# Kernel optimization log

Measured on AMD Instinct MI355X. Metric: run time of the kernel, lower is better.

The kernel has to match this reference:

```python
import jax, jax.numpy as jnp
import numpy as np

IMG, P, C = 512, 16, 1
D, DEPTH, H, DH, MLP = 768, 12, 8, 64, 2048
GRID = IMG // P          # 32
NP = GRID * GRID         # 1024 patches
N = NP + 1               # +cls token
EPS = 1e-5


def _ln(x, s, b):
    m = jnp.mean(x, -1, keepdims=True)
    v = jnp.mean((x - m) ** 2, -1, keepdims=True)
    return (x - m) * jax.lax.rsqrt(v + EPS) * s + b


def setup_inputs() -> dict:
    key = jax.random.key(0)
    ks = jax.random.split(key, 12)
    s = 0.02
    f32 = jnp.float32
    return {
        "x": jax.random.normal(ks[0], (4, C, IMG, IMG), f32),
        "conv_w": jax.random.normal(ks[1], (D, C, P, P), f32) * s,   # [out,in,kh,kw] like torch
        "conv_b": jnp.zeros((D,), f32),
        "cls_token": jax.random.normal(ks[2], (1, 1, D), f32),
        "pos_emb": jax.random.normal(ks[3], (1, N, D), f32),
        "qkv_w": jax.random.normal(ks[4], (DEPTH, D, 3 * H * DH), f32) * s,  # [in,out] layout
        "merge_w": jax.random.normal(ks[5], (DEPTH, H * DH, D), f32) * s,
        "merge_b": jnp.zeros((DEPTH, D), f32),
        "ln1_s": jnp.ones((DEPTH, D), f32),
        "ln1_b": jnp.zeros((DEPTH, D), f32),
        "ln2_s": jnp.ones((DEPTH, D), f32),
        "ln2_b": jnp.zeros((DEPTH, D), f32),
        "ffn_w1": jax.random.normal(ks[6], (DEPTH, D, MLP), f32) * s,
        "ffn_b1": jnp.zeros((DEPTH, MLP), f32),
        "ffn_w2": jax.random.normal(ks[7], (DEPTH, MLP, D), f32) * s,
        "ffn_b2": jnp.zeros((DEPTH, D), f32),
        "lnf_s": jnp.ones((D,), f32),
        "lnf_b": jnp.zeros((D,), f32),
    }


def reference(x, conv_w, conv_b, cls_token, pos_emb, qkv_w, merge_w, merge_b,
              ln1_s, ln1_b, ln2_s, ln2_b, ffn_w1, ffn_b1, ffn_w2, ffn_b2,
              lnf_s, lnf_b):
    B = x.shape[0]
    # Patch embed: stride-P conv == non-overlapping patch extraction + matmul
    xr = x.reshape(B, C, GRID, P, GRID, P)
    tok = jnp.einsum('bchpwq,dcpq->bhwd', xr, conv_w).reshape(B, NP, D) + conv_b
    t = jnp.concatenate([jnp.broadcast_to(cls_token, (B, 1, D)), tok], axis=1)
    t = t + pos_emb  # dropout is identity in eval
    scale = DH ** -0.5
    for i in range(DEPTH):
        # MSA with pre-LN
        h = _ln(t, ln1_s[i], ln1_b[i])
        qkv = (h @ qkv_w[i]).reshape(B, N, H, 3, DH)   # [B,N,H,3,DH]
        q = jnp.transpose(qkv[..., 0, :], (0, 2, 1, 3))  # [B,H,N,DH]
        k = jnp.transpose(qkv[..., 1, :], (0, 2, 1, 3))
        v = jnp.transpose(qkv[..., 2, :], (0, 2, 1, 3))
        att = jax.nn.softmax(jnp.einsum('bhnd,bhmd->bhnm', q, k) * scale, axis=-1)
        o = jnp.einsum('bhnm,bhmd->bhnd', att, v)
        o = jnp.transpose(o, (0, 2, 1, 3)).reshape(B, N, H * DH)
        t = t + (o @ merge_w[i] + merge_b[i])
        # FFN with pre-LN, exact (erf) GELU like torch nn.GELU
        h2 = _ln(t, ln2_s[i], ln2_b[i])
        f = jax.nn.gelu(h2 @ ffn_w1[i] + ffn_b1[i], approximate=False)
        t = t + (f @ ffn_w2[i] + ffn_b2[i])
    return _ln(t, lnf_s, lnf_b)
```

## Files before the change

kernel.cpp:

```cpp
#include <hip/hip_runtime.h>

#define DEV __device__ __forceinline__

typedef short s8v __attribute__((ext_vector_type(8)));
typedef float f4v __attribute__((ext_vector_type(4)));
typedef unsigned int u32x2 __attribute__((ext_vector_type(2)));

DEV short f2bf(float f) {
  unsigned u = __float_as_uint(f);
  u += 0x7FFFu + ((u >> 16) & 1u);
  return (short)(u >> 16);
}
DEV short f2bf_fast(float f) {
  return (short)((__float_as_uint(f) + 0x8000u) >> 16);
}
DEV float bf2f(short s) { return __uint_as_float(((unsigned)(unsigned short)s) << 16); }

DEV void gld_lds16(const short* g, short* l) {
  __builtin_amdgcn_global_load_lds(
      (const __attribute__((address_space(1))) void*)g,
      (__attribute__((address_space(3))) void*)l, 16, 0, 0);
}

DEV u32x2 trr(unsigned lds_byte) {
  u32x2 r;
  asm volatile("ds_read_b64_tr_b16 %0, %1" : "=&v"(r) : "v"(lds_byte));
  return r;
}

DEV int xcd_swz(int id, int nwg) {
  int q8 = nwg >> 3, r8 = nwg & 7, xcd = id & 7, off = id >> 3;
  return (xcd < r8) ? (xcd * (q8 + 1) + off) : (r8 * (q8 + 1) + (xcd - r8) * q8 + off);
}

template<int BN>
__global__ __launch_bounds__(256) void gemm_t(
    const short* __restrict__ A, const short* __restrict__ B, void* __restrict__ Cv,
    const float* __restrict__ bias,
    int M, int N, int K, int lda, int ldb, int ldc, int flags)
{
  constexpr int BPASS = BN / 32;
  constexpr int MI = (BN == 128) ? 4 : 2;
  __shared__ __align__(16) short As[2][64 * 64];
  __shared__ __align__(16) short Bs[2][BN * 64];
  int nwg = gridDim.x * gridDim.y;
  int idl = blockIdx.y * gridDim.x + blockIdx.x;
  int swz = xcd_swz(idl, nwg);
  int bx = swz % gridDim.x, by = swz / gridDim.x;
  int m0 = by * 64, n0 = bx * BN;
  int tid = threadIdx.x, lane = tid & 63, w = tid >> 6;
  int lr = lane & 15, kg = lane >> 4;
  int wrb = (BN == 128) ? 0 : (w >> 1) * 32;
  int wcb = (BN == 128) ? w * 32 : (w & 1) * 32;
  f4v acc[MI][2] = {};
  int NT = K >> 6;

#define STAGE(bufi, k0)                                                   \
  {                                                                       \
    _Pragma("unroll")                                                     \
    for (int p = 0; p < 2; ++p) {                                         \
      int ch = p * 256 + w * 64 + lane;                                   \
      int row = ch >> 3, c = (ch & 7) ^ (row & 7);                        \
      gld_lds16(A + (long)(m0 + row) * lda + (k0) + c * 8,                \
                &As[bufi][(p * 256 + w * 64) * 8]);                       \
    }                                                                     \
    _Pragma("unroll")                                                     \
    for (int p = 0; p < BPASS; ++p) {                                     \
      int ch = p * 256 + w * 64 + lane;                                   \
      int row = ch >> 3, c = (ch & 7) ^ (row & 7);                        \
      gld_lds16(B + (long)(n0 + row) * ldb + (k0) + c * 8,                \
                &Bs[bufi][(p * 256 + w * 64) * 8]);                       \
    }                                                                     \
  }

  STAGE(0, 0)
  for (int t = 0; t < NT; ++t) {
    int buf = t & 1;
    if (t + 1 < NT) {
      STAGE(buf ^ 1, (t + 1) * 64)
      if constexpr (BN == 128)
        asm volatile("s_waitcnt vmcnt(6)" ::: "memory");
      else
        asm volatile("s_waitcnt vmcnt(4)" ::: "memory");
    } else {
      asm volatile("s_waitcnt vmcnt(0)" ::: "memory");
    }
    __builtin_amdgcn_s_barrier();
    #pragma unroll
    for (int ks = 0; ks < 2; ++ks) {
      s8v av[MI], bv[2];
      #pragma unroll
      for (int mi = 0; mi < MI; ++mi) {
        int row = wrb + mi * 16 + lr;
        int sl = (ks * 4 + kg) ^ (row & 7);
        av[mi] = *(const s8v*)&As[buf][row * 64 + sl * 8];
      }
      #pragma unroll
      for (int ni = 0; ni < 2; ++ni) {
        int row = wcb + ni * 16 + lr;
        int sl = (ks * 4 + kg) ^ (row & 7);
        bv[ni] = *(const s8v*)&Bs[buf][row * 64 + sl * 8];
      }
      #pragma unroll
      for (int mi = 0; mi < MI; ++mi)
        #pragma unroll
        for (int ni = 0; ni < 2; ++ni)
          acc[mi][ni] = __builtin_amdgcn_mfma_f32_16x16x32_bf16(av[mi], bv[ni], acc[mi][ni], 0, 0, 0);
    }
    asm volatile("s_waitcnt lgkmcnt(0)" ::: "memory");
    __builtin_amdgcn_s_barrier();
  }
#undef STAGE

  float* Cf = (float*)Cv;
  short* Cb = (short*)Cv;
  #pragma unroll
  for (int mi = 0; mi < MI; ++mi)
    #pragma unroll
    for (int ni = 0; ni < 2; ++ni) {
      int col = n0 + wcb + ni * 16 + lr;
      float bvv = (flags & 1) ? bias[col] : 0.f;
      #pragma unroll
      for (int j = 0; j < 4; ++j) {
        int row = m0 + wrb + mi * 16 + kg * 4 + j;
        if (row >= M) continue;
        float v = acc[mi][ni][j] + bvv;
        if (flags & 2) v = 0.5f * v * (1.f + erff(v * 0.70710678118f));
        long ci = (long)row * ldc + col;
        if (flags & 8) Cb[ci] = f2bf(v);
        else { if (flags & 4) v += Cf[ci]; Cf[ci] = v; }
      }
    }
}

__global__ __launch_bounds__(256) void flash_k(
    const short* __restrict__ qkv, float* __restrict__ Opart, float* __restrict__ ML)
{
  int swz = xcd_swz(blockIdx.x, 1088);
  int h = swz / 544, rem = swz - h * 544;
  int z = rem / 17, qt = rem - z * 17;
  int zb = z >> 3, zh = z & 7;
  const short* base = qkv + (long)zb * 1025 * 1536 + zh * 192;
  const short* Qg = base;
  const short* Kg = base + 64;
  const short* Vg = base + 128;
  int q0 = qt * 64;
  int kt0 = h * 8;
  int tid = threadIdx.x, lane = tid & 63, w = tid >> 6;
  int lr = lane & 15, kg = lane >> 4;

  __shared__ __align__(16) short Ks[2][64 * 64];
  __shared__ __align__(16) short Vs[2][64 * 64];

  s8v aq[2];
  {
    long qrow = q0 + w * 16 + lr;
    aq[0] = *(const s8v*)(Qg + qrow * 1536 + kg * 8);
    aq[1] = *(const s8v*)(Qg + qrow * 1536 + 32 + kg * 8);
  }

  unsigned vsbase = (unsigned)(unsigned long long)
      (__attribute__((address_space(3))) void*)&Vs[0][0];
  unsigned vtr = (unsigned)(lr * 8 + kg * 1024);

#define STAGE_K(bufi, kv0)                                                 \
  {                                                                        \
    int s0 = w * 128;                                                      \
    _Pragma("unroll")                                                      \
    for (int i = 0; i < 2; ++i) {                                          \
      int s = s0 + i * 64 + lane;                                          \
      int row = s >> 3, c = (s & 7) ^ (row & 7);                           \
      gld_lds16(Kg + (long)((kv0) + row) * 1536 + c * 8,                   \
                &Ks[bufi][(s0 + i * 64) * 8]);                             \
    }                                                                      \
  }
#define STAGE_V(bufi, kv0)                                                 \
  {                                                                        \
    int s0 = w * 128;                                                      \
    _Pragma("unroll")                                                      \
    for (int i = 0; i < 2; ++i) {                                          \
      int ch = s0 + i * 64 + lane;                                         \
      int st = ch >> 3, r = (ch & 7) >> 1, hh = ch & 1;                    \
      int key = (kv0) + (st >> 2) * 4 + r;                                 \
      int d = (st & 3) * 16 + hh * 8;                                      \
      gld_lds16(Vg + (long)key * 1536 + d,                                 \
                &Vs[bufi][(s0 + i * 64) * 8]);                             \
    }                                                                      \
  }

  f4v acc[4] = {};
  float m_run = -3.0e38f, l_run = 0.f;
  const float C2 = 0.18033688011112042f;
  const float THR = 44.36f;

  STAGE_K(0, kt0 * 64)
  STAGE_V(0, kt0 * 64)
  asm volatile("s_waitcnt vmcnt(0)" ::: "memory");
  __builtin_amdgcn_s_barrier();

  for (int kt = kt0; kt < kt0 + 8; ++kt) {
    int cur = (kt - kt0) & 1;
    if (kt + 1 < kt0 + 8) {
      STAGE_K(cur ^ 1, (kt + 1) * 64)
      STAGE_V(cur ^ 1, (kt + 1) * 64)
    }

    f4v sa[4] = {};
    __builtin_amdgcn_s_setprio(1);
    #pragma unroll
    for (int ni = 0; ni < 4; ++ni) {
      int row = ni * 16 + lr;
      #pragma unroll
      for (int ks = 0; ks < 2; ++ks) {
        int c = (ks * 4 + kg) ^ (row & 7);
        s8v kf = *(const s8v*)&Ks[cur][row * 64 + c * 8];
        sa[ni] = __builtin_amdgcn_mfma_f32_16x16x32_bf16(kf, aq[ks], sa[ni], 0, 0, 0);
      }
    }
    __builtin_amdgcn_s_setprio(0);

    float tm = -3.0e38f;
    #pragma unroll
    for (int ni = 0; ni < 4; ++ni)
      #pragma unroll
      for (int jj = 0; jj < 4; ++jj) tm = fmaxf(tm, sa[ni][jj]);
    tm = fmaxf(tm, __shfl_xor(tm, 16));
    tm = fmaxf(tm, __shfl_xor(tm, 32));
    bool need = !__all(tm <= m_run + THR);
    float scale = 1.f;
    if (need) {
      float m_new = fmaxf(m_run, tm);
      scale = exp2f((m_run - m_new) * C2);
      m_run = m_new;
    }
    float mC = m_run * C2;
    float pv[4][4];
    float ts = 0.f;
    #pragma unroll
    for (int ni = 0; ni < 4; ++ni)
      #pragma unroll
      for (int jj = 0; jj < 4; ++jj) {
        float p = exp2f(fmaf(sa[ni][jj], C2, -mC));
        pv[ni][jj] = p;
        ts += p;
      }
    ts += __shfl_xor(ts, 16);
    ts += __shfl_xor(ts, 32);
    l_run = l_run * scale + ts;
    if (need) {
      float scq[4];
      #pragma unroll
      for (int jj = 0; jj < 4; ++jj)
        scq[jj] = __shfl(scale, kg * 4 + jj + 16 * kg);
      #pragma unroll
      for (int ni = 0; ni < 4; ++ni)
        #pragma unroll
        for (int jj = 0; jj < 4; ++jj) acc[ni][jj] *= scq[jj];
    }

    unsigned pr[4][2];
    #pragma unroll
    for (int ni = 0; ni < 4; ++ni)
      #pragma unroll
      for (int hh = 0; hh < 2; ++hh) {
        unsigned lo = (unsigned)(unsigned short)f2bf_fast(pv[ni][2 * hh]);
        unsigned hi = (unsigned)(unsigned short)f2bf_fast(pv[ni][2 * hh + 1]);
        pr[ni][hh] = lo | (hi << 16);
      }
    union PU { s8v v; unsigned u[4]; };
    PU apu[2];
    #pragma unroll
    for (int ks = 0; ks < 2; ++ks)
      #pragma unroll
      for (int t = 0; t < 4; ++t) {
        unsigned src = (kg & 2) ? pr[2 * ks + 1][t & 1] : pr[2 * ks][t & 1];
        apu[ks].u[t] = __shfl(src, lr + 16 * (2 * (kg & 1) + (t >> 1)));
      }

    u32x2 tr[4][2][2];
    unsigned vb = vsbase + (unsigned)cur * 8192u + vtr;
    #pragma unroll
    for (int ni = 0; ni < 4; ++ni)
      #pragma unroll
      for (int ks = 0; ks < 2; ++ks) {
        tr[ni][ks][0] = trr(vb + ni * 128 + ks * 4096);
        tr[ni][ks][1] = trr(vb + ni * 128 + ks * 4096 + 512);
      }
    asm volatile("s_waitcnt lgkmcnt(0)" ::: "memory");
    __builtin_amdgcn_sched_barrier(0);

    __builtin_amdgcn_s_setprio(1);
    #pragma unroll
    for (int ni = 0; ni < 4; ++ni) {
      #pragma unroll
      for (int ks = 0; ks < 2; ++ks) {
        union { s8v v; u32x2 u2[2]; } bb;
        bb.u2[0] = tr[ni][ks][0];
        bb.u2[1] = tr[ni][ks][1];
        acc[ni] = __builtin_amdgcn_mfma_f32_16x16x32_bf16(apu[ks].v, bb.v, acc[ni], 0, 0, 0);
      }
    }
    __builtin_amdgcn_s_setprio(0);
    asm volatile("s_waitcnt lgkmcnt(0)" ::: "memory");
    asm volatile("s_waitcnt vmcnt(0)" ::: "memory");
    __builtin_amdgcn_s_barrier();
  }
#undef STAGE_K
#undef STAGE_V

  if (h) {
    s8v k0 = *(const s8v*)(Kg + 1024L * 1536 + kg * 8);
    s8v k1 = *(const s8v*)(Kg + 1024L * 1536 + 32 + kg * 8);
    float s = 0.f;
    #pragma unroll
    for (int j = 0; j < 8; ++j)
      s += bf2f(aq[0][j]) * bf2f(k0[j]) + bf2f(aq[1][j]) * bf2f(k1[j]);
    s += __shfl_xor(s, 16);
    s += __shfl_xor(s, 32);
    float m_new = fmaxf(m_run, s);
    float sc = exp2f((m_run - m_new) * C2);
    float p = exp2f((s - m_new) * C2);
    m_run = m_new;
    l_run = l_run * sc + p;
    float vrow[4];
    #pragma unroll
    for (int ni = 0; ni < 4; ++ni)
      vrow[ni] = bf2f(Vg[1024L * 1536 + ni * 16 + lr]);
    float scq[4], pq[4];
    #pragma unroll
    for (int jj = 0; jj < 4; ++jj) {
      scq[jj] = __shfl(sc, kg * 4 + jj + 16 * kg);
      pq[jj]  = __shfl(p,  kg * 4 + jj + 16 * kg);
    }
    #pragma unroll
    for (int ni = 0; ni < 4; ++ni)
      #pragma unroll
      for (int jj = 0; jj < 4; ++jj)
        acc[ni][jj] = acc[ni][jj] * scq[jj] + pq[jj] * vrow[ni];
  }

  long zrow = (long)(h * 32 + z) * 1025;
  if (kg == 0) {
    int row = q0 + w * 16 + lr;
    if (row < 1025) {
      ML[(zrow + row) * 2]     = m_run * C2;
      ML[(zrow + row) * 2 + 1] = l_run;
    }
  }
  #pragma unroll
  for (int ni = 0; ni < 4; ++ni)
    #pragma unroll
    for (int jj = 0; jj < 4; ++jj) {
      int row = q0 + w * 16 + kg * 4 + jj;
      if (row < 1025)
        Opart[(zrow + row) * 64 + ni * 16 + lr] = acc[ni][jj];
    }
}

__global__ __launch_bounds__(256) void fcomb_k(
    const float* __restrict__ Opart, const float* __restrict__ ML, short* __restrict__ O)
{
  int idx = blockIdx.x * 256 + threadIdx.x;
  int d = idx & 63;
  int r = idx >> 6;
  int z = r / 1025, row = r - z * 1025;
  float m0 = ML[(long)r * 2], l0 = ML[(long)r * 2 + 1];
  float m1 = ML[(long)(32800 + r) * 2], l1 = ML[(long)(32800 + r) * 2 + 1];
  float M = fmaxf(m0, m1);
  float w0 = exp2f(m0 - M), w1 = exp2f(m1 - M);
  float inv = 1.f / (l0 * w0 + l1 * w1);
  float v = (Opart[(long)r * 64 + d] * w0 + Opart[(long)(32800 + r) * 64 + d] * w1) * inv;
  int zb = z >> 3, zh = z & 7;
  O[((long)(zb * 1025 + row)) * 512 + zh * 64 + d] = f2bf(v);
}

DEV void tconv_body(const float* w, short* wt, int K, int N, int bx, int by, int tid)
{
  __shared__ float tile[32][33];
  int n0 = bx * 32, k0 = by * 32;
  int tx = tid & 31, ty = tid >> 5;
  #pragma unroll
  for (int j = 0; j < 4; ++j)
    tile[ty + j * 8][tx] = w[(long)(k0 + ty + j * 8) * N + n0 + tx];
  __syncthreads();
  #pragma unroll
  for (int j = 0; j < 4; ++j)
    wt[(long)(n0 + ty + j * 8) * K + k0 + tx] = f2bf(tile[tx][ty + j * 8]);
}

__global__ __launch_bounds__(256) void tconv4_k(
    const float* __restrict__ sq, const float* __restrict__ sm,
    const float* __restrict__ sf1, const float* __restrict__ sf2,
    short* __restrict__ dq, short* __restrict__ dm,
    short* __restrict__ df1, short* __restrict__ df2)
{
  int id = blockIdx.x, tid = threadIdx.x;
  if (id < 1152)       tconv_body(sq,  dq,  768, 1536, id % 48,          id / 48,          tid);
  else if (id < 1536)  tconv_body(sm,  dm,  512, 768,  (id - 1152) % 24, (id - 1152) / 24, tid);
  else if (id < 3072)  tconv_body(sf1, df1, 768, 2048, (id - 1536) % 64, (id - 1536) / 64, tid);
  else                 tconv_body(sf2, df2, 2048, 768, (id - 3072) % 24, (id - 3072) / 24, tid);
}

__global__ __launch_bounds__(256) void cvt_k(const float* __restrict__ in,
    short* __restrict__ out, int n)
{
  int i = blockIdx.x * 256 + threadIdx.x;
  if (i < n) out[i] = f2bf(in[i]);
}

DEV void st_ln(float* p, float v) { *p = v; }
DEV void st_ln(short* p, float v) { *p = f2bf(v); }

template<typename OT>
__global__ __launch_bounds__(256) void ln_k(const float* __restrict__ x,
    const float* __restrict__ g, const float* __restrict__ b,
    OT* __restrict__ y, int rows)
{
  int row = blockIdx.x;
  if (row >= rows) return;
  const float* xr = x + (long)row * 768;
  OT* yr = y + (long)row * 768;
  int t = threadIdx.x;
  float v0 = xr[t], v1 = xr[t + 256], v2 = xr[t + 512];
  float s = v0 + v1 + v2, s2 = v0 * v0 + v1 * v1 + v2 * v2;
  #pragma unroll
  for (int o = 32; o > 0; o >>= 1) { s += __shfl_down(s, o); s2 += __shfl_down(s2, o); }
  __shared__ float as_[4], as2_[4];
  if ((t & 63) == 0) { as_[t >> 6] = s; as2_[t >> 6] = s2; }
  __syncthreads();
  s = as_[0] + as_[1] + as_[2] + as_[3];
  s2 = as2_[0] + as2_[1] + as2_[2] + as2_[3];
  float mean = s * (1.f / 768.f);
  float var = s2 * (1.f / 768.f) - mean * mean;
  float r = rsqrtf(var + 1e-5f);
  st_ln(&yr[t],       (v0 - mean) * r * g[t]       + b[t]);
  st_ln(&yr[t + 256], (v1 - mean) * r * g[t + 256] + b[t + 256]);
  st_ln(&yr[t + 512], (v2 - mean) * r * g[t + 512] + b[t + 512]);
}

__global__ __launch_bounds__(256) void im2col_k(const float* __restrict__ x,
    short* __restrict__ A)
{
  int i = blockIdx.x * 256 + threadIdx.x;
  int k = i & 255, row = i >> 8;
  int px = k & 15, py = k >> 4;
  int gx = row & 31, gy = (row >> 5) & 31, b = row >> 10;
  A[i] = f2bf(x[((long)(b * 512) + gy * 16 + py) * 512 + gx * 16 + px]);
}

__global__ __launch_bounds__(256) void assemble_k(const short* __restrict__ tok,
    const float* __restrict__ cls, const float* __restrict__ pos, float* __restrict__ t)
{
  int i = blockIdx.x * 256 + threadIdx.x;
  int d = i % 768; int rn = i / 768; int n = rn % 1025; int b = rn / 1025;
  float v = (n == 0) ? cls[d] : bf2f(tok[((long)(b * 1024 + n - 1)) * 768 + d]);
  t[i] = v + pos[n * 768 + d];
}

extern "C" void kernel_launch(void* const* d_in, const int* in_sizes, int n_in,
                              void* d_out, int out_size, void* d_ws, size_t ws_size,
                              hipStream_t stream)
{
  const float* x       = (const float*)d_in[0];
  const float* conv_w  = (const float*)d_in[1];
  const float* conv_b  = (const float*)d_in[2];
  const float* cls     = (const float*)d_in[3];
  const float* pos     = (const float*)d_in[4];
  const float* qkv_w   = (const float*)d_in[5];
  const float* merge_w = (const float*)d_in[6];
  const float* merge_b = (const float*)d_in[7];
  const float* ln1_s   = (const float*)d_in[8];
  const float* ln1_b   = (const float*)d_in[9];
  const float* ln2_s   = (const float*)d_in[10];
  const float* ln2_b   = (const float*)d_in[11];
  const float* ffn_w1  = (const float*)d_in[12];
  const float* ffn_b1  = (const float*)d_in[13];
  const float* ffn_w2  = (const float*)d_in[14];
  const float* ffn_b2  = (const float*)d_in[15];
  const float* lnf_s   = (const float*)d_in[16];
  const float* lnf_b   = (const float*)d_in[17];

  char* wsp = (char*)d_ws;
  size_t o = 0;
  auto take = [&](size_t bytes) { char* r = wsp + o; o = (o + bytes + 255) & ~(size_t)255; return r; };
  short* wq   = (short*)take(1536ul * 768 * 2);
  short* wm   = (short*)take(768ul * 512 * 2);
  short* wf1  = (short*)take(2048ul * 768 * 2);
  short* wf2  = (short*)take(768ul * 2048 * 2);
  short* wcv  = (short*)take(768ul * 256 * 2);
  float* t    = (float*)take(4100ul * 768 * 4);
  char*  hO   = take(4352ul * 768 * 2);
  short* qkv  = (short*)take(4ul * 1025 * 1536 * 2);
  char*  fV   = take(4352ul * 2048 * 2);
  take(2ul << 20);

  short* h     = (short*)hO;
  short* O     = (short*)hO;
  short* f     = (short*)fV;
  short* imc   = (short*)fV;
  short* tok   = (short*)(fV + 4096ul * 256 * 2);
  float* Opart = (float*)fV;
  float* ML    = (float*)(fV + 16793600);

  dim3 blk(256);

  cvt_k<<<768, blk, 0, stream>>>(conv_w, wcv, 768 * 256);
  im2col_k<<<4096, blk, 0, stream>>>(x, imc);
  gemm_t<64><<<dim3(12, 64), blk, 0, stream>>>(imc, wcv, tok, conv_b,
      4096, 768, 256, 256, 256, 768, 1 | 8);
  assemble_k<<<12300, blk, 0, stream>>>(tok, cls, pos, t);

  for (int i = 0; i < 12; ++i) {
    tconv4_k<<<4608, blk, 0, stream>>>(
        qkv_w + (long)i * 768 * 1536, merge_w + (long)i * 512 * 768,
        ffn_w1 + (long)i * 768 * 2048, ffn_w2 + (long)i * 2048 * 768,
        wq, wm, wf1, wf2);

    ln_k<short><<<4100, blk, 0, stream>>>(t, ln1_s + i * 768, ln1_b + i * 768, h, 4100);
    gemm_t<64><<<dim3(24, 65), blk, 0, stream>>>(h, wq, qkv, nullptr,
        4100, 1536, 768, 768, 768, 1536, 8);
    flash_k<<<1088, blk, 0, stream>>>(qkv, Opart, ML);
    fcomb_k<<<8200, blk, 0, stream>>>(Opart, ML, O);
    gemm_t<64><<<dim3(12, 65), blk, 0, stream>>>(O, wm, t, merge_b + i * 768,
        4100, 768, 512, 512, 512, 768, 1 | 4);
    ln_k<short><<<4100, blk, 0, stream>>>(t, ln2_s + i * 768, ln2_b + i * 768, h, 4100);
    gemm_t<64><<<dim3(32, 65), blk, 0, stream>>>(h, wf1, f, ffn_b1 + i * 2048,
        4100, 2048, 768, 768, 768, 2048, 1 | 2 | 8);
    gemm_t<64><<<dim3(12, 65), blk, 0, stream>>>(f, wf2, t, ffn_b2 + i * 768,
        4100, 768, 2048, 2048, 2048, 768, 1 | 4);
  }
  ln_k<float><<<4100, blk, 0, stream>>>(t, lnf_s, lnf_b, (float*)d_out, 4100);
}
```

Measured before the change: 2.034 ms.

## Fuse split-KV flash combine into one 512-thread block; vectorize layernorm per wave

The flash attention kernel now runs both KV halves as two 4-wave groups inside one 512-thread block. The partial accumulators and max/sum statistics are merged through LDS, and bf16 output is written directly. This removes the separate fcomb kernel and the fp32 Opart/ML round-trip through global memory. Separately, layernorm processes one row per wave with float4 loads and shuffle-only reductions, removing the shared-memory barrier. The costs are a doubled LDS footprint per block and an extra block-wide barrier before the combine.

```diff
diff --git a/kernel.cpp b/kernel.cpp
--- a/kernel.cpp
+++ b/kernel.cpp
@@ -2,6 +2,7 @@
 
 #define DEV __device__ __forceinline__
 
+typedef short s4v __attribute__((ext_vector_type(4)));
 typedef short s8v __attribute__((ext_vector_type(8)));
 typedef float f4v __attribute__((ext_vector_type(4)));
 typedef unsigned int u32x2 __attribute__((ext_vector_type(2)));
@@ -133,50 +134,50 @@
     }
 }
 
-__global__ __launch_bounds__(256) void flash_k(
-    const short* __restrict__ qkv, float* __restrict__ Opart, float* __restrict__ ML)
-{
-  int swz = xcd_swz(blockIdx.x, 1088);
-  int h = swz / 544, rem = swz - h * 544;
-  int z = rem / 17, qt = rem - z * 17;
+__global__ __launch_bounds__(512) void flash_k(
+    const short* __restrict__ qkv, short* __restrict__ O)
+{
+  int swz = xcd_swz(blockIdx.x, 544);
+  int z = swz / 17, qt = swz - z * 17;
   int zb = z >> 3, zh = z & 7;
   const short* base = qkv + (long)zb * 1025 * 1536 + zh * 192;
   const short* Qg = base;
   const short* Kg = base + 64;
   const short* Vg = base + 128;
   int q0 = qt * 64;
-  int kt0 = h * 8;
   int tid = threadIdx.x, lane = tid & 63, w = tid >> 6;
+  int g = w >> 2, wl = w & 3;
   int lr = lane & 15, kg = lane >> 4;
-
-  __shared__ __align__(16) short Ks[2][64 * 64];
-  __shared__ __align__(16) short Vs[2][64 * 64];
+  int kt0 = g * 8;
+
+  __shared__ __align__(16) short Ks[2][2][64 * 64];
+  __shared__ __align__(16) short Vs[2][2][64 * 64];
 
   s8v aq[2];
   {
-    long qrow = q0 + w * 16 + lr;
+    long qrow = q0 + wl * 16 + lr;
     aq[0] = *(const s8v*)(Qg + qrow * 1536 + kg * 8);
     aq[1] = *(const s8v*)(Qg + qrow * 1536 + 32 + kg * 8);
   }
 
   unsigned vsbase = (unsigned)(unsigned long long)
-      (__attribute__((address_space(3))) void*)&Vs[0][0];
+      (__attribute__((address_space(3))) void*)&Vs[0][0][0];
   unsigned vtr = (unsigned)(lr * 8 + kg * 1024);
 
 #define STAGE_K(bufi, kv0)                                                 \
   {                                                                        \
-    int s0 = w * 128;                                                      \
+    int s0 = wl * 128;                                                     \
     _Pragma("unroll")                                                      \
     for (int i = 0; i < 2; ++i) {                                          \
       int s = s0 + i * 64 + lane;                                          \
       int row = s >> 3, c = (s & 7) ^ (row & 7);                           \
       gld_lds16(Kg + (long)((kv0) + row) * 1536 + c * 8,                   \
-                &Ks[bufi][(s0 + i * 64) * 8]);                             \
+                &Ks[g][bufi][(s0 + i * 64) * 8]);                          \
     }                                                                      \
   }
 #define STAGE_V(bufi, kv0)                                                 \
   {                                                                        \
-    int s0 = w * 128;                                                      \
+    int s0 = wl * 128;                                                     \
     _Pragma("unroll")                                                      \
     for (int i = 0; i < 2; ++i) {                                          \
       int ch = s0 + i * 64 + lane;                                         \
@@ -184,7 +185,7 @@
       int key = (kv0) + (st >> 2) * 4 + r;                                 \
       int d = (st & 3) * 16 + hh * 8;                                      \
       gld_lds16(Vg + (long)key * 1536 + d,                                 \
-                &Vs[bufi][(s0 + i * 64) * 8]);                             \
+                &Vs[g][bufi][(s0 + i * 64) * 8]);                          \
     }                                                                      \
   }
 
@@ -213,7 +214,7 @@
       #pragma unroll
       for (int ks = 0; ks < 2; ++ks) {
         int c = (ks * 4 + kg) ^ (row & 7);
-        s8v kf = *(const s8v*)&Ks[cur][row * 64 + c * 8];
+        s8v kf = *(const s8v*)&Ks[g][cur][row * 64 + c * 8];
         sa[ni] = __builtin_amdgcn_mfma_f32_16x16x32_bf16(kf, aq[ks], sa[ni], 0, 0, 0);
       }
     }
@@ -278,7 +279,7 @@
       }
 
     u32x2 tr[4][2][2];
-    unsigned vb = vsbase + (unsigned)cur * 8192u + vtr;
+    unsigned vb = vsbase + (unsigned)(g * 2 + cur) * 8192u + vtr;
     #pragma unroll
     for (int ni = 0; ni < 4; ++ni)
       #pragma unroll
@@ -308,7 +309,7 @@
 #undef STAGE_K
 #undef STAGE_V
 
-  if (h) {
+  if (g) {
     s8v k0 = *(const s8v*)(Kg + 1024L * 1536 + kg * 8);
     s8v k1 = *(const s8v*)(Kg + 1024L * 1536 + 32 + kg * 8);
     float s = 0.f;
@@ -339,39 +340,45 @@
         acc[ni][jj] = acc[ni][jj] * scq[jj] + pq[jj] * vrow[ni];
   }
 
-  long zrow = (long)(h * 32 + z) * 1025;
+  float* AccL = (float*)&Ks[0][0][0];
+  float* MLs  = (float*)&Vs[0][0][0];
   if (kg == 0) {
-    int row = q0 + w * 16 + lr;
-    if (row < 1025) {
-      ML[(zrow + row) * 2]     = m_run * C2;
-      ML[(zrow + row) * 2 + 1] = l_run;
-    }
-  }
-  #pragma unroll
-  for (int ni = 0; ni < 4; ++ni)
+    MLs[(g * 64 + wl * 16 + lr) * 2]     = m_run;
+    MLs[(g * 64 + wl * 16 + lr) * 2 + 1] = l_run;
+  }
+  if (g == 0) {
+    #pragma unroll
+    for (int ni = 0; ni < 4; ++ni)
+      #pragma unroll
+      for (int jj = 0; jj < 4; ++jj)
+        AccL[(wl * 16 + kg * 4 + jj) * 64 + ni * 16 + lr] = acc[ni][jj];
+  }
+  asm volatile("s_waitcnt lgkmcnt(0)" ::: "memory");
+  __builtin_amdgcn_s_barrier();
+  if (g == 1) {
+    float m0 = MLs[(wl * 16 + lr) * 2], l0 = MLs[(wl * 16 + lr) * 2 + 1];
+    float M = fmaxf(m0, m_run);
+    float w0 = exp2f((m0 - M) * C2), w1 = exp2f((m_run - M) * C2);
+    float inv = 1.f / (l0 * w0 + l_run * w1);
+    float c0 = w0 * inv, c1 = w1 * inv;
+    float c0q[4], c1q[4];
     #pragma unroll
     for (int jj = 0; jj < 4; ++jj) {
-      int row = q0 + w * 16 + kg * 4 + jj;
-      if (row < 1025)
-        Opart[(zrow + row) * 64 + ni * 16 + lr] = acc[ni][jj];
-    }
-}
-
-__global__ __launch_bounds__(256) void fcomb_k(
-    const float* __restrict__ Opart, const float* __restrict__ ML, short* __restrict__ O)
-{
-  int idx = blockIdx.x * 256 + threadIdx.x;
-  int d = idx & 63;
-  int r = idx >> 6;
-  int z = r / 1025, row = r - z * 1025;
-  float m0 = ML[(long)r * 2], l0 = ML[(long)r * 2 + 1];
-  float m1 = ML[(long)(32800 + r) * 2], l1 = ML[(long)(32800 + r) * 2 + 1];
-  float M = fmaxf(m0, m1);
-  float w0 = exp2f(m0 - M), w1 = exp2f(m1 - M);
-  float inv = 1.f / (l0 * w0 + l1 * w1);
-  float v = (Opart[(long)r * 64 + d] * w0 + Opart[(long)(32800 + r) * 64 + d] * w1) * inv;
-  int zb = z >> 3, zh = z & 7;
-  O[((long)(zb * 1025 + row)) * 512 + zh * 64 + d] = f2bf(v);
+      c0q[jj] = __shfl(c0, kg * 4 + jj + 16 * kg);
+      c1q[jj] = __shfl(c1, kg * 4 + jj + 16 * kg);
+    }
+    #pragma unroll
+    for (int ni = 0; ni < 4; ++ni)
+      #pragma unroll
+      for (int jj = 0; jj < 4; ++jj) {
+        int row = q0 + wl * 16 + kg * 4 + jj;
+        if (row < 1025) {
+          float a0 = AccL[(wl * 16 + kg * 4 + jj) * 64 + ni * 16 + lr];
+          O[((long)(zb * 1025 + row)) * 512 + zh * 64 + ni * 16 + lr] =
+              f2bf(a0 * c0q[jj] + acc[ni][jj] * c1q[jj]);
+        }
+      }
+  }
 }
 
 DEV void tconv_body(const float* w, short* wt, int K, int N, int bx, int by, int tid)
@@ -408,34 +415,44 @@
   if (i < n) out[i] = f2bf(in[i]);
 }
 
-DEV void st_ln(float* p, float v) { *p = v; }
-DEV void st_ln(short* p, float v) { *p = f2bf(v); }
+DEV void st4(float* p, f4v v) { *(f4v*)p = v; }
+DEV void st4(short* p, f4v v) {
+  s4v o = { f2bf(v[0]), f2bf(v[1]), f2bf(v[2]), f2bf(v[3]) };
+  *(s4v*)p = o;
+}
 
 template<typename OT>
 __global__ __launch_bounds__(256) void ln_k(const float* __restrict__ x,
     const float* __restrict__ g, const float* __restrict__ b,
     OT* __restrict__ y, int rows)
 {
-  int row = blockIdx.x;
+  int row = blockIdx.x * 4 + (threadIdx.x >> 6);
   if (row >= rows) return;
+  int lane = threadIdx.x & 63;
   const float* xr = x + (long)row * 768;
-  OT* yr = y + (long)row * 768;
-  int t = threadIdx.x;
-  float v0 = xr[t], v1 = xr[t + 256], v2 = xr[t + 512];
-  float s = v0 + v1 + v2, s2 = v0 * v0 + v1 * v1 + v2 * v2;
-  #pragma unroll
-  for (int o = 32; o > 0; o >>= 1) { s += __shfl_down(s, o); s2 += __shfl_down(s2, o); }
-  __shared__ float as_[4], as2_[4];
-  if ((t & 63) == 0) { as_[t >> 6] = s; as2_[t >> 6] = s2; }
-  __syncthreads();
-  s = as_[0] + as_[1] + as_[2] + as_[3];
-  s2 = as2_[0] + as2_[1] + as2_[2] + as2_[3];
+  f4v v[3];
+  #pragma unroll
+  for (int i = 0; i < 3; ++i) v[i] = *(const f4v*)(xr + i * 256 + lane * 4);
+  float s = 0.f, s2 = 0.f;
+  #pragma unroll
+  for (int i = 0; i < 3; ++i)
+    #pragma unroll
+    for (int j = 0; j < 4; ++j) { s += v[i][j]; s2 += v[i][j] * v[i][j]; }
+  #pragma unroll
+  for (int o = 1; o < 64; o <<= 1) { s += __shfl_xor(s, o); s2 += __shfl_xor(s2, o); }
   float mean = s * (1.f / 768.f);
   float var = s2 * (1.f / 768.f) - mean * mean;
   float r = rsqrtf(var + 1e-5f);
-  st_ln(&yr[t],       (v0 - mean) * r * g[t]       + b[t]);
-  st_ln(&yr[t + 256], (v1 - mean) * r * g[t + 256] + b[t + 256]);
-  st_ln(&yr[t + 512], (v2 - mean) * r * g[t + 512] + b[t + 512]);
+  OT* yr = y + (long)row * 768;
+  #pragma unroll
+  for (int i = 0; i < 3; ++i) {
+    f4v gg = *(const f4v*)(g + i * 256 + lane * 4);
+    f4v bb = *(const f4v*)(b + i * 256 + lane * 4);
+    f4v o;
+    #pragma unroll
+    for (int j = 0; j < 4; ++j) o[j] = (v[i][j] - mean) * r * gg[j] + bb[j];
+    st4(yr + i * 256 + lane * 4, o);
+  }
 }
 
 __global__ __launch_bounds__(256) void im2col_k(const float* __restrict__ x,
@@ -494,15 +511,13 @@
   char*  fV   = take(4352ul * 2048 * 2);
   take(2ul << 20);
 
-  short* h     = (short*)hO;
-  short* O     = (short*)hO;
-  short* f     = (short*)fV;
-  short* imc   = (short*)fV;
-  short* tok   = (short*)(fV + 4096ul * 256 * 2);
-  float* Opart = (float*)fV;
-  float* ML    = (float*)(fV + 16793600);
-
-  dim3 blk(256);
+  short* h   = (short*)hO;
+  short* O   = (short*)hO;
+  short* f   = (short*)fV;
+  short* imc = (short*)fV;
+  short* tok = (short*)(fV + 4096ul * 256 * 2);
+
+  dim3 blk(256), blk512(512);
 
   cvt_k<<<768, blk, 0, stream>>>(conv_w, wcv, 768 * 256);
   im2col_k<<<4096, blk, 0, stream>>>(x, imc);
@@ -516,18 +531,17 @@
         ffn_w1 + (long)i * 768 * 2048, ffn_w2 + (long)i * 2048 * 768,
         wq, wm, wf1, wf2);
 
-    ln_k<short><<<4100, blk, 0, stream>>>(t, ln1_s + i * 768, ln1_b + i * 768, h, 4100);
+    ln_k<short><<<1025, blk, 0, stream>>>(t, ln1_s + i * 768, ln1_b + i * 768, h, 4100);
     gemm_t<64><<<dim3(24, 65), blk, 0, stream>>>(h, wq, qkv, nullptr,
         4100, 1536, 768, 768, 768, 1536, 8);
-    flash_k<<<1088, blk, 0, stream>>>(qkv, Opart, ML);
-    fcomb_k<<<8200, blk, 0, stream>>>(Opart, ML, O);
+    flash_k<<<544, blk512, 0, stream>>>(qkv, O);
     gemm_t<64><<<dim3(12, 65), blk, 0, stream>>>(O, wm, t, merge_b + i * 768,
         4100, 768, 512, 512, 512, 768, 1 | 4);
-    ln_k<short><<<4100, blk, 0, stream>>>(t, ln2_s + i * 768, ln2_b + i * 768, h, 4100);
+    ln_k<short><<<1025, blk, 0, stream>>>(t, ln2_s + i * 768, ln2_b + i * 768, h, 4100);
     gemm_t<64><<<dim3(32, 65), blk, 0, stream>>>(h, wf1, f, ffn_b1 + i * 2048,
         4100, 2048, 768, 768, 768, 2048, 1 | 2 | 8);
     gemm_t<64><<<dim3(12, 65), blk, 0, stream>>>(f, wf2, t, ffn_b2 + i * 768,
         4100, 768, 2048, 2048, 2048, 768, 1 | 4);
   }
-  ln_k<float><<<4100, blk, 0, stream>>>(t, lnf_s, lnf_b, (float*)d_out, 4100);
-}
+  ln_k<float><<<1025, blk, 0, stream>>>(t, lnf_s, lnf_b, (float*)d_out, 4100);
+}
```

New measurement: 1.969 ms. 1.03x faster.
